# Optimization experiments

Hardware: AMD Instinct MI355X
Metric: run time of the kernel (lower is better)

## Reference

```python
import jax, jax.numpy as jnp
import numpy as np

NEG_SLOPE = 0.2


def gat_layer(x, src, dst, W, a_src, a_dst, bias, num_nodes, concat):
    """PyG-style GATConv (eval mode, self-loops already included in src/dst).
    x: [N, F_in]; W: [F_in, H*C]; a_src, a_dst: [H, C]; bias: [H*C] or [C].
    """
    H, C = a_src.shape
    h = (x @ W).reshape(num_nodes, H, C)                    # [N,H,C]
    alpha_s = jnp.einsum('nhc,hc->nh', h, a_src)            # [N,H]
    alpha_d = jnp.einsum('nhc,hc->nh', h, a_dst)            # [N,H]
    e = alpha_s[src] + alpha_d[dst]                         # [E,H]
    e = jnp.where(e > 0, e, NEG_SLOPE * e)                  # LeakyReLU(0.2)
    # segment softmax over destination nodes (numerically stable)
    m = jax.ops.segment_max(e, dst, num_segments=num_nodes)  # [N,H]
    m = jnp.where(jnp.isfinite(m), m, 0.0)
    ex = jnp.exp(e - m[dst])                                # [E,H]
    s = jax.ops.segment_sum(ex, dst, num_segments=num_nodes)  # [N,H]
    alpha = ex / (s[dst] + 1e-16)                           # [E,H]
    msg = h[src] * alpha[:, :, None]                        # [E,H,C]
    out = jax.ops.segment_sum(msg, dst, num_segments=num_nodes)  # [N,H,C]
    if concat:
        out = out.reshape(num_nodes, H * C)
    else:
        out = out.mean(axis=1)
    return out + bias


def _forward(x, edge_index, W1, a_src1, a_dst1, b1, W2, a_src2, a_dst2, b2):
    N = x.shape[0]
    loops = jnp.arange(N, dtype=edge_index.dtype)
    src = jnp.concatenate([edge_index[0], loops])
    dst = jnp.concatenate([edge_index[1], loops])
    h = gat_layer(x, src, dst, W1, a_src1, a_dst1, b1, N, concat=True)
    h = jax.nn.relu(h)  # dropout inactive in eval
    h = gat_layer(h, src, dst, W2, a_src2, a_dst2, b2, N, concat=False)
    return jax.nn.log_softmax(h, axis=1)


def setup_inputs() -> dict:
    key = jax.random.key(0)
    ks = jax.random.split(key, 10)
    N, E, F_in, Hid, H1, F_out = 100000, 1600000, 128, 64, 2, 7
    x = jax.random.normal(ks[0], (N, F_in), dtype=jnp.float32)
    edge_index = jax.random.randint(ks[1], (2, E), 0, N, dtype=jnp.int64)
    s1 = 1.0 / np.sqrt(F_in)
    W1 = jax.random.uniform(ks[2], (F_in, H1 * Hid), jnp.float32, -s1, s1)
    a_src1 = jax.random.uniform(ks[3], (H1, Hid), jnp.float32, -s1, s1)
    a_dst1 = jax.random.uniform(ks[4], (H1, Hid), jnp.float32, -s1, s1)
    b1 = jnp.zeros((H1 * Hid,), jnp.float32)
    s2 = 1.0 / np.sqrt(H1 * Hid)
    W2 = jax.random.uniform(ks[5], (H1 * Hid, F_out), jnp.float32, -s2, s2)
    a_src2 = jax.random.uniform(ks[6], (1, F_out), jnp.float32, -s2, s2)
    a_dst2 = jax.random.uniform(ks[7], (1, F_out), jnp.float32, -s2, s2)
    b2 = jnp.zeros((F_out,), jnp.float32)
    return {"x": x, "edge_index": edge_index, "W1": W1, "a_src1": a_src1,
            "a_dst1": a_dst1, "b1": b1, "W2": W2, "a_src2": a_src2,
            "a_dst2": a_dst2, "b2": b2}


def reference(x, edge_index, W1, a_src1, a_dst1, b1, W2, a_src2, a_dst2, b2):
    return _forward(x, edge_index, W1, a_src1, a_dst1, b1, W2, a_src2, a_dst2, b2)
```

## Files before the change

### kernel.cpp

```cpp
#include <hip/hip_runtime.h>
#include <hip/hip_bf16.h>

#define F_IN 128
#define HC   128
#define C1   64
#define F_OUT 7
#define H2S  8
#define BSH  9
#define BSZ  512
#define BINCH 8192
#define BCAP 12288

typedef __attribute__((ext_vector_type(8))) short short8;
typedef __attribute__((ext_vector_type(4))) float f32x4;
typedef __attribute__((ext_vector_type(2))) float f32x2;

__device__ __forceinline__ ushort f2bf(float f) {
    uint u = __builtin_bit_cast(uint, f);
    u = (u + 0x7FFFu + ((u >> 16) & 1u)) >> 16;
    return (ushort)u;
}

__device__ __forceinline__ int perm_col(int p_byte) {
    int slp = p_byte >> 3, j = p_byte & 7;
    int h = slp >> 3, sg = slp & 7;
    int lr = 2 * sg + (j >> 2), jj = j & 3;
    return 16 * (4 * h + jj) + lr;
}

__global__ __launch_bounds__(256) void k_bincvt(
    const int* __restrict__ ei, int E, int Etot, int NBIN,
    int* __restrict__ bcnt, uint* __restrict__ binned,
    const float* __restrict__ W1, ushort* __restrict__ Wsw,
    const float* __restrict__ W2, const float* __restrict__ b1,
    float* __restrict__ W2p, float* __restrict__ b1p)
{
    int b = blockIdx.x, t = threadIdx.x;
    if (b < NBIN) {
        __shared__ int hist[256];
        __shared__ int base[256];
        hist[t] = 0;
        __syncthreads();
        long c0 = (long)b * BINCH;
#pragma unroll
        for (int i = 0; i < BINCH / 256; ++i) {
            long e = c0 + t + i * 256;
            if (e < Etot) {
                int d = (e < E) ? ei[E + e] : (int)(e - E);
                atomicAdd(&hist[d >> BSH], 1);
            }
        }
        __syncthreads();
        base[t] = t * BCAP + ((hist[t] > 0) ? atomicAdd(&bcnt[t], hist[t]) : 0);
        __syncthreads();
#pragma unroll
        for (int i = 0; i < BINCH / 256; ++i) {
            long e = c0 + t + i * 256;
            if (e < Etot) {
                int s, d;
                if (e < E) { s = ei[e]; d = ei[E + e]; } else { s = (int)(e - E); d = s; }
                int bkt = d >> BSH;
                int pos = atomicAdd(&base[bkt], 1);
                if (pos < (bkt + 1) * BCAP)
                    binned[pos] = ((uint)s << BSH) | (uint)(d & (BSZ - 1));
            }
        }
    } else if (b < NBIN + 64) {
        int i = (b - NBIN) * 256 + t;
        int k = i >> 7, n = i & 127;
        float v = W1[k * HC + n];
        int idx = n * 128 + (((k & ~7) ^ ((n & 7) << 3)) | (k & 7));
        Wsw[idx] = f2bf(v);
    } else {
        for (int i = t; i < 128 * F_OUT; i += 256) {
            int p = i / F_OUT, o = i - p * F_OUT;
            W2p[i] = W2[perm_col(p) * F_OUT + o];
        }
        if (t < 128) b1p[t] = b1[perm_col(t)];
    }
}

__global__ __launch_bounds__(256) void k_fillgemm(
    const uint* __restrict__ binned, const int* __restrict__ bcnt,
    int* __restrict__ rowptr, int* __restrict__ csr,
    const float* __restrict__ x, const ushort* __restrict__ Wsw,
    const float* __restrict__ a_src, const float* __restrict__ a_dst,
    unsigned char* __restrict__ h1p, float* __restrict__ as1, float* __restrict__ ad1,
    int N, int NB)
{
    __shared__ __align__(16) char smem[128 * 128 * 2];
    const int t = threadIdx.x;

    if ((int)blockIdx.x < NB) {
        int* deg = (int*)smem;
        int* cur = deg + BSZ;
        int* sc  = cur + BSZ;
        int b = blockIdx.x;
        int cv = (t < NB) ? min(bcnt[t], BCAP) : 0;
        sc[t] = cv;
        __syncthreads();
        for (int off = 1; off < 256; off <<= 1) {
            int u = (t >= off) ? sc[t - off] : 0;
            __syncthreads();
            sc[t] += u;
            __syncthreads();
        }
        int total = sc[255];
        int s0 = (b > 0) ? sc[b - 1] : 0;
        int cntb = min(bcnt[b], BCAP);
        __syncthreads();

        int n0 = b << BSH;
        int nn = N - n0; if (nn > BSZ) nn = BSZ;
        deg[t] = 0; deg[t + 256] = 0;
        __syncthreads();
        const uint* bb = binned + (size_t)b * BCAP;
        for (int i = t; i < cntb; i += 256)
            atomicAdd(&deg[bb[i] & (BSZ - 1)], 1);
        __syncthreads();
        int d0 = deg[2 * t], d1 = deg[2 * t + 1];
        int ts = d0 + d1;
        sc[t] = ts;
        __syncthreads();
        for (int off = 1; off < 256; off <<= 1) {
            int u = (t >= off) ? sc[t - off] : 0;
            __syncthreads();
            sc[t] += u;
            __syncthreads();
        }
        int ex = sc[t] - ts + s0;
        if (2 * t < nn)     { rowptr[n0 + 2 * t]     = ex;      cur[2 * t]     = ex; }
        if (2 * t + 1 < nn) { rowptr[n0 + 2 * t + 1] = ex + d0; cur[2 * t + 1] = ex + d0; }
        __syncthreads();
        for (int i = t; i < cntb; i += 256) {
            uint en = bb[i];
            int pos = atomicAdd(&cur[en & (BSZ - 1)], 1);
            csr[pos] = (int)(en >> BSH);
        }
        if (b == 0 && t == 0) rowptr[N] = total;
    } else {
        ushort* Bs = (ushort*)smem;
        const int w = t >> 6, l = t & 63;
        const int lr = l & 15, hi = l >> 4;
        const int n0 = (blockIdx.x - NB) * 64;

        {
            const uint4* src = (const uint4*)Wsw;
            uint4* dst = (uint4*)Bs;
#pragma unroll
            for (int it = 0; it < 8; ++it) dst[t + it * 256] = src[t + it * 256];
        }
        __syncthreads();

        f32x4 acc[8];
#pragma unroll
        for (int j = 0; j < 8; ++j) acc[j] = (f32x4){0.f, 0.f, 0.f, 0.f};

        int arow = n0 + w * 16 + lr;
        if (arow >= N) arow = N - 1;
        const float* aptr = x + (size_t)arow * F_IN + hi * 8;

#pragma unroll
        for (int kt = 0; kt < 4; ++kt) {
            float4 f0 = *(const float4*)(aptr + kt * 32);
            float4 f1 = *(const float4*)(aptr + kt * 32 + 4);
            short8 a;
            a[0] = (short)f2bf(f0.x); a[1] = (short)f2bf(f0.y);
            a[2] = (short)f2bf(f0.z); a[3] = (short)f2bf(f0.w);
            a[4] = (short)f2bf(f1.x); a[5] = (short)f2bf(f1.y);
            a[6] = (short)f2bf(f1.z); a[7] = (short)f2bf(f1.w);
#pragma unroll
            for (int j = 0; j < 8; ++j) {
                int rn = 16 * j + lr;
                int kidx = (kt * 32 + hi * 8) ^ ((rn & 7) << 3);
                short8 b = *(const short8*)(Bs + rn * 128 + kidx);
                acc[j] = __builtin_amdgcn_mfma_f32_16x16x32_bf16(a, b, acc[j], 0, 0, 0);
            }
        }

        float as_[8], ad_[8];
#pragma unroll
        for (int j = 0; j < 8; ++j) {
            int hd = j >> 2;
            int c = 16 * (j & 3) + lr;
            as_[j] = a_src[hd * C1 + c];
            ad_[j] = a_dst[hd * C1 + c];
        }
#pragma unroll
        for (int i = 0; i < 4; ++i) {
            int r = n0 + w * 16 + hi * 4 + i;
            float ps0 = 0, ps1 = 0, pd0 = 0, pd1 = 0;
#pragma unroll
            for (int j = 0; j < 4; ++j) { ps0 += acc[j][i] * as_[j]; pd0 += acc[j][i] * ad_[j]; }
#pragma unroll
            for (int j = 4; j < 8; ++j) { ps1 += acc[j][i] * as_[j]; pd1 += acc[j][i] * ad_[j]; }
#pragma unroll
            for (int off = 1; off <= 8; off <<= 1) {
                ps0 += __shfl_xor(ps0, off, 64);
                ps1 += __shfl_xor(ps1, off, 64);
                pd0 += __shfl_xor(pd0, off, 64);
                pd1 += __shfl_xor(pd1, off, 64);
            }
            if (r < N) {
                int w0 = 0, w1 = 0;
                w0 = __builtin_amdgcn_cvt_pk_fp8_f32(acc[0][i], acc[1][i], w0, false);
                w0 = __builtin_amdgcn_cvt_pk_fp8_f32(acc[2][i], acc[3][i], w0, true);
                w1 = __builtin_amdgcn_cvt_pk_fp8_f32(acc[4][i], acc[5][i], w1, false);
                w1 = __builtin_amdgcn_cvt_pk_fp8_f32(acc[6][i], acc[7][i], w1, true);
                *(uint*)(h1p + (size_t)r * HC + lr * 4)      = (uint)w0;
                *(uint*)(h1p + (size_t)r * HC + 64 + lr * 4) = (uint)w1;
                if (lr == 0) {
                    as1[r * 2 + 0] = ps0; as1[r * 2 + 1] = ps1;
                    ad1[r * 2 + 0] = pd0; ad1[r * 2 + 1] = pd1;
                }
            }
        }
    }
}

__global__ __launch_bounds__(256) void k_aggr1_l2(
    const int* __restrict__ rowptr, const int* __restrict__ csr_src,
    const float* __restrict__ as1, const float* __restrict__ ad1,
    const unsigned char* __restrict__ h1p, const float* __restrict__ b1p,
    const float* __restrict__ W2p, const float* __restrict__ a_src2,
    const float* __restrict__ a_dst2,
    float* __restrict__ h2p, float* __restrict__ as2, float* __restrict__ ad2,
    int N)
{
    int w = threadIdx.x >> 6, l = threadIdx.x & 63;
    int q = l >> 4, sl = l & 15;
    int n = blockIdx.x * 16 + w * 4 + q;
    if (n >= N) return;
    const int h = sl >> 3;
    const int boff = sl * 8;
    float adv = ad1[n * 2 + h];
    int beg = rowptr[n], end = rowptr[n + 1];
    f32x2 ac01 = {0.f, 0.f}, ac23 = {0.f, 0.f}, ac45 = {0.f, 0.f}, ac67 = {0.f, 0.f};
    float s = 0.f;

    int i = beg;
    for (; i + 4 <= end; i += 4) {
        int sv[4]; float Av[4]; uint2 Hv[4];
#pragma unroll
        for (int j = 0; j < 4; ++j) sv[j] = csr_src[i + j];
#pragma unroll
        for (int j = 0; j < 4; ++j) Av[j] = as1[sv[j] * 2 + h];
#pragma unroll
        for (int j = 0; j < 4; ++j)
            Hv[j] = *(const uint2*)(h1p + (((size_t)(uint)sv[j]) << 7) + boff);
#pragma unroll
        for (int j = 0; j < 4; ++j) {
            float a = Av[j] + adv; a = a > 0.f ? a : 0.2f * a;
            float e = __expf(a);
            s += e;
            f32x2 ev = {e, e};
            ac01 += ev * __builtin_amdgcn_cvt_pk_f32_fp8((int)Hv[j].x, false);
            ac23 += ev * __builtin_amdgcn_cvt_pk_f32_fp8((int)Hv[j].x, true);
            ac45 += ev * __builtin_amdgcn_cvt_pk_f32_fp8((int)Hv[j].y, false);
            ac67 += ev * __builtin_amdgcn_cvt_pk_f32_fp8((int)Hv[j].y, true);
        }
    }
    for (; i < end; ++i) {
        int src = csr_src[i];
        float a = as1[src * 2 + h] + adv; a = a > 0.f ? a : 0.2f * a;
        float e = __expf(a);
        s += e;
        uint2 hv = *(const uint2*)(h1p + (((size_t)(uint)src) << 7) + boff);
        f32x2 ev = {e, e};
        ac01 += ev * __builtin_amdgcn_cvt_pk_f32_fp8((int)hv.x, false);
        ac23 += ev * __builtin_amdgcn_cvt_pk_f32_fp8((int)hv.x, true);
        ac45 += ev * __builtin_amdgcn_cvt_pk_f32_fp8((int)hv.y, false);
        ac67 += ev * __builtin_amdgcn_cvt_pk_f32_fp8((int)hv.y, true);
    }
    float inv = 1.f / (s + 1e-16f);

    float4 bv0 = *(const float4*)&b1p[sl * 8];
    float4 bv1 = *(const float4*)&b1p[sl * 8 + 4];
    float v[8];
    v[0] = fmaxf(ac01[0] * inv + bv0.x, 0.f);
    v[1] = fmaxf(ac01[1] * inv + bv0.y, 0.f);
    v[2] = fmaxf(ac23[0] * inv + bv0.z, 0.f);
    v[3] = fmaxf(ac23[1] * inv + bv0.w, 0.f);
    v[4] = fmaxf(ac45[0] * inv + bv1.x, 0.f);
    v[5] = fmaxf(ac45[1] * inv + bv1.y, 0.f);
    v[6] = fmaxf(ac67[0] * inv + bv1.z, 0.f);
    v[7] = fmaxf(ac67[1] * inv + bv1.w, 0.f);

    float w2r[56];
    {
        const float4* wp = (const float4*)(W2p + sl * 56);
#pragma unroll
        for (int k = 0; k < 14; ++k) {
            float4 f = wp[k];
            w2r[4 * k + 0] = f.x; w2r[4 * k + 1] = f.y;
            w2r[4 * k + 2] = f.z; w2r[4 * k + 3] = f.w;
        }
    }
    float p[7];
#pragma unroll
    for (int j = 0; j < 7; ++j) p[j] = 0.f;
#pragma unroll
    for (int r = 0; r < 8; ++r)
#pragma unroll
        for (int j = 0; j < 7; ++j) p[j] += v[r] * w2r[r * 7 + j];
#pragma unroll
    for (int off = 1; off <= 8; off <<= 1)
#pragma unroll
        for (int j = 0; j < 7; ++j) p[j] += __shfl_xor(p[j], off, 64);

    if (sl == 0) {
        float asv = 0.f, adv2 = 0.f;
#pragma unroll
        for (int j = 0; j < 7; ++j) {
            h2p[(size_t)n * H2S + j] = p[j];
            asv += p[j] * a_src2[j];
            adv2 += p[j] * a_dst2[j];
        }
        h2p[(size_t)n * H2S + 7] = 0.f;
        as2[n] = asv; ad2[n] = adv2;
    }
}

__global__ __launch_bounds__(256) void k_aggr2ls(
    const int* __restrict__ rowptr, const int* __restrict__ csr_src,
    const float* __restrict__ as2, const float* __restrict__ ad2,
    const float* __restrict__ h2p, const float* __restrict__ b2,
    float* __restrict__ out, int N)
{
    int g = blockIdx.x * blockDim.x + threadIdx.x;
    int n = g >> 2, l = g & 3;
    if (n >= N) return;
    float adv = ad2[n];
    int beg = rowptr[n], end = rowptr[n + 1];
    f32x2 acc = {0.f, 0.f};
    float s = 0.f;
    int i = beg;
    for (; i + 4 <= end; i += 4) {
        int sv[4]; float Av[4]; float2 Hv[4];
#pragma unroll
        for (int j = 0; j < 4; ++j) sv[j] = csr_src[i + j];
#pragma unroll
        for (int j = 0; j < 4; ++j) Av[j] = as2[sv[j]];
#pragma unroll
        for (int j = 0; j < 4; ++j)
            Hv[j] = *(const float2*)(h2p + ((size_t)(uint)sv[j]) * H2S + 2 * l);
#pragma unroll
        for (int j = 0; j < 4; ++j) {
            float a = Av[j] + adv;
            a = a > 0.f ? a : 0.2f * a;
            float e = __expf(a);
            s += e;
            f32x2 ev = {e, e};
            f32x2 hv = {Hv[j].x, Hv[j].y};
            acc += ev * hv;
        }
    }
    for (; i < end; ++i) {
        int s0 = csr_src[i];
        float a = as2[s0] + adv;
        a = a > 0.f ? a : 0.2f * a;
        float e = __expf(a);
        s += e;
        float2 hv2 = *(const float2*)(h2p + ((size_t)(uint)s0) * H2S + 2 * l);
        f32x2 ev = {e, e};
        f32x2 hv = {hv2.x, hv2.y};
        acc += ev * hv;
    }
    float invs = 1.f / (s + 1e-16f);
    float va = acc[0] * invs + b2[2 * l];
    float vb = (2 * l + 1 < 7) ? acc[1] * invs + b2[2 * l + 1] : -1e30f;
    float m = fmaxf(va, vb);
#pragma unroll
    for (int off = 1; off <= 2; off <<= 1)
        m = fmaxf(m, __shfl_xor(m, off, 4));
    float ex = __expf(va - m) + ((2 * l + 1 < 7) ? __expf(vb - m) : 0.f);
#pragma unroll
    for (int off = 1; off <= 2; off <<= 1)
        ex += __shfl_xor(ex, off, 4);
    float lg = __logf(ex);
    out[(size_t)n * F_OUT + 2 * l] = va - m - lg;
    if (2 * l + 1 < 7) out[(size_t)n * F_OUT + 2 * l + 1] = vb - m - lg;
}

extern "C" void kernel_launch(void* const* d_in, const int* in_sizes, int n_in,
                              void* d_out, int out_size, void* d_ws, size_t ws_size,
                              hipStream_t stream) {
    const float* x      = (const float*)d_in[0];
    const int*   ei     = (const int*)d_in[1];
    const float* W1     = (const float*)d_in[2];
    const float* a_src1 = (const float*)d_in[3];
    const float* a_dst1 = (const float*)d_in[4];
    const float* b1     = (const float*)d_in[5];
    const float* W2     = (const float*)d_in[6];
    const float* a_src2 = (const float*)d_in[7];
    const float* a_dst2 = (const float*)d_in[8];
    const float* b2     = (const float*)d_in[9];
    float* out = (float*)d_out;

    const int N    = in_sizes[0] / F_IN;
    const int E    = in_sizes[1] / 2;
    const int Etot = E + N;
    const int NB   = (N + BSZ - 1) >> BSH;
    const int NBIN = (Etot + BINCH - 1) / BINCH;

    char* ws = (char*)d_ws;
    size_t off = 0;
    auto A = [&](size_t bytes) -> void* {
        char* p = ws + off;
        off += (bytes + 255) & ~(size_t)255;
        return (void*)p;
    };
    ushort* Wsw    = (ushort*)A((size_t)128 * 128 * 2);
    float*  W2p    = (float*) A((size_t)128 * F_OUT * 4);
    float*  b1p    = (float*) A((size_t)128 * 4);
    unsigned char* h1p = (unsigned char*)A((size_t)N * HC);
    float*  as1    = (float*) A((size_t)N * 2 * 4);
    float*  ad1    = (float*) A((size_t)N * 2 * 4);
    int*    rowptr = (int*)   A((size_t)(N + 1) * 4);
    int*    csr    = (int*)   A((size_t)Etot * 4);
    int*    bcnt   = (int*)   A(256 * 4);
    uint*   binned = (uint*)  A((size_t)NB * BCAP * 4);
    float*  h2p    = (float*)binned;
    float*  as2    = (float*)((char*)binned + (((size_t)N * H2S * 4 + 255) & ~(size_t)255));
    float*  ad2    = (float*)((char*)as2 + (((size_t)N * 4 + 255) & ~(size_t)255));

    hipMemsetAsync(bcnt, 0, 256 * 4, stream);

    k_bincvt<<<NBIN + 65, 256, 0, stream>>>(ei, E, Etot, NBIN, bcnt, binned,
                                            W1, Wsw, W2, b1, W2p, b1p);
    k_fillgemm<<<NB + (N + 63) / 64, 256, 0, stream>>>(
        binned, bcnt, rowptr, csr,
        x, Wsw, a_src1, a_dst1, h1p, as1, ad1, N, NB);
    k_aggr1_l2<<<(N + 15) / 16, 256, 0, stream>>>(rowptr, csr, as1, ad1, h1p,
                                                  b1p, W2p, a_src2, a_dst2,
                                                  h2p, as2, ad2, N);
    k_aggr2ls<<<((size_t)N * 4 + 255) / 256, 256, 0, stream>>>(rowptr, csr, as2, ad2,
                                                               h2p, b2, out, N);
}
```

Measured before the change: 147.5 us.

## Sort destination nodes by degree to balance aggregation warps

Builds a degree histogram while constructing the CSR, then a new kernel counting-sorts node ids by in-degree into an order array. Both aggregation kernels process nodes in that order, so the 16-lane groups within a wave handle nodes of similar degree and lose less time to divergent loop lengths. This adds an extra kernel launch, an indirect lookup per node, and scattered writes of outputs that no longer follow node order.

```diff
diff --git a/kernel.cpp b/kernel.cpp
--- a/kernel.cpp
+++ b/kernel.cpp
@@ -10,6 +10,7 @@
 #define BSZ  512
 #define BINCH 8192
 #define BCAP 12288
+#define DBIN 64
 
 typedef __attribute__((ext_vector_type(8))) short short8;
 typedef __attribute__((ext_vector_type(4))) float f32x4;
@@ -82,7 +83,7 @@
 
 __global__ __launch_bounds__(256) void k_fillgemm(
     const uint* __restrict__ binned, const int* __restrict__ bcnt,
-    int* __restrict__ rowptr, int* __restrict__ csr,
+    int* __restrict__ rowptr, int* __restrict__ csr, int* __restrict__ dhist,
     const float* __restrict__ x, const ushort* __restrict__ Wsw,
     const float* __restrict__ a_src, const float* __restrict__ a_dst,
     unsigned char* __restrict__ h1p, float* __restrict__ as1, float* __restrict__ ad1,
@@ -95,9 +96,11 @@
         int* deg = (int*)smem;
         int* cur = deg + BSZ;
         int* sc  = cur + BSZ;
+        int* ldh = sc + 256;
         int b = blockIdx.x;
         int cv = (t < NB) ? min(bcnt[t], BCAP) : 0;
         sc[t] = cv;
+        if (t < DBIN) ldh[t] = 0;
         __syncthreads();
         for (int off = 1; off < 256; off <<= 1) {
             int u = (t >= off) ? sc[t - off] : 0;
@@ -129,9 +132,12 @@
             __syncthreads();
         }
         int ex = sc[t] - ts + s0;
-        if (2 * t < nn)     { rowptr[n0 + 2 * t]     = ex;      cur[2 * t]     = ex; }
-        if (2 * t + 1 < nn) { rowptr[n0 + 2 * t + 1] = ex + d0; cur[2 * t + 1] = ex + d0; }
-        __syncthreads();
+        if (2 * t < nn)     { rowptr[n0 + 2 * t]     = ex;      cur[2 * t]     = ex;
+                              atomicAdd(&ldh[min(d0, DBIN - 1)], 1); }
+        if (2 * t + 1 < nn) { rowptr[n0 + 2 * t + 1] = ex + d0; cur[2 * t + 1] = ex + d0;
+                              atomicAdd(&ldh[min(d1, DBIN - 1)], 1); }
+        __syncthreads();
+        if (t < DBIN && ldh[t]) atomicAdd(&dhist[t], ldh[t]);
         for (int i = t; i < cntb; i += 256) {
             uint en = bb[i];
             int pos = atomicAdd(&cur[en & (BSZ - 1)], 1);
@@ -218,7 +224,38 @@
     }
 }
 
+__global__ __launch_bounds__(256) void k_order(
+    const int* __restrict__ rowptr, const int* __restrict__ dhist,
+    int* __restrict__ dcur, int* __restrict__ order, int N)
+{
+    __shared__ int dstart[DBIN];
+    __shared__ int lh[DBIN];
+    __shared__ int lbase[DBIN];
+    __shared__ int lcur[DBIN];
+    int t = threadIdx.x;
+    if (t == 0) {
+        int a = 0;
+        for (int i = 0; i < DBIN; ++i) { dstart[i] = a; a += dhist[i]; }
+    }
+    if (t < DBIN) { lh[t] = 0; lcur[t] = 0; }
+    __syncthreads();
+    int n = blockIdx.x * 256 + t;
+    int d = -1;
+    if (n < N) {
+        d = min(rowptr[n + 1] - rowptr[n], DBIN - 1);
+        atomicAdd(&lh[d], 1);
+    }
+    __syncthreads();
+    if (t < DBIN && lh[t]) lbase[t] = atomicAdd(&dcur[t], lh[t]);
+    __syncthreads();
+    if (n < N) {
+        int p = atomicAdd(&lcur[d], 1);
+        order[dstart[d] + lbase[d] + p] = n;
+    }
+}
+
 __global__ __launch_bounds__(256) void k_aggr1_l2(
+    const int* __restrict__ order,
     const int* __restrict__ rowptr, const int* __restrict__ csr_src,
     const float* __restrict__ as1, const float* __restrict__ ad1,
     const unsigned char* __restrict__ h1p, const float* __restrict__ b1p,
@@ -229,8 +266,9 @@
 {
     int w = threadIdx.x >> 6, l = threadIdx.x & 63;
     int q = l >> 4, sl = l & 15;
-    int n = blockIdx.x * 16 + w * 4 + q;
-    if (n >= N) return;
+    int idx = blockIdx.x * 16 + w * 4 + q;
+    if (idx >= N) return;
+    int n = order[idx];
     const int h = sl >> 3;
     const int boff = sl * 8;
     float adv = ad1[n * 2 + h];
@@ -322,14 +360,16 @@
 }
 
 __global__ __launch_bounds__(256) void k_aggr2ls(
+    const int* __restrict__ order,
     const int* __restrict__ rowptr, const int* __restrict__ csr_src,
     const float* __restrict__ as2, const float* __restrict__ ad2,
     const float* __restrict__ h2p, const float* __restrict__ b2,
     float* __restrict__ out, int N)
 {
     int g = blockIdx.x * blockDim.x + threadIdx.x;
-    int n = g >> 2, l = g & 3;
-    if (n >= N) return;
+    int idx = g >> 2, l = g & 3;
+    if (idx >= N) return;
+    int n = order[idx];
     float adv = ad2[n];
     int beg = rowptr[n], end = rowptr[n + 1];
     f32x2 acc = {0.f, 0.f};
@@ -418,22 +458,27 @@
     float*  ad1    = (float*) A((size_t)N * 2 * 4);
     int*    rowptr = (int*)   A((size_t)(N + 1) * 4);
     int*    csr    = (int*)   A((size_t)Etot * 4);
-    int*    bcnt   = (int*)   A(256 * 4);
+    int*    order  = (int*)   A((size_t)N * 4);
+    int*    misc   = (int*)   A((256 + DBIN + DBIN) * 4);
+    int*    bcnt   = misc;
+    int*    dhist  = misc + 256;
+    int*    dcur   = misc + 256 + DBIN;
     uint*   binned = (uint*)  A((size_t)NB * BCAP * 4);
     float*  h2p    = (float*)binned;
     float*  as2    = (float*)((char*)binned + (((size_t)N * H2S * 4 + 255) & ~(size_t)255));
     float*  ad2    = (float*)((char*)as2 + (((size_t)N * 4 + 255) & ~(size_t)255));
 
-    hipMemsetAsync(bcnt, 0, 256 * 4, stream);
+    hipMemsetAsync(misc, 0, (256 + DBIN + DBIN) * 4, stream);
 
     k_bincvt<<<NBIN + 65, 256, 0, stream>>>(ei, E, Etot, NBIN, bcnt, binned,
                                             W1, Wsw, W2, b1, W2p, b1p);
     k_fillgemm<<<NB + (N + 63) / 64, 256, 0, stream>>>(
-        binned, bcnt, rowptr, csr,
+        binned, bcnt, rowptr, csr, dhist,
         x, Wsw, a_src1, a_dst1, h1p, as1, ad1, N, NB);
-    k_aggr1_l2<<<(N + 15) / 16, 256, 0, stream>>>(rowptr, csr, as1, ad1, h1p,
+    k_order<<<(N + 255) / 256, 256, 0, stream>>>(rowptr, dhist, dcur, order, N);
+    k_aggr1_l2<<<(N + 15) / 16, 256, 0, stream>>>(order, rowptr, csr, as1, ad1, h1p,
                                                   b1p, W2p, a_src2, a_dst2,
                                                   h2p, as2, ad2, N);
-    k_aggr2ls<<<((size_t)N * 4 + 255) / 256, 256, 0, stream>>>(rowptr, csr, as2, ad2,
-                                                               h2p, b2, out, N);
-}
+    k_aggr2ls<<<((size_t)N * 4 + 255) / 256, 256, 0, stream>>>(order, rowptr, csr,
+                                                               as2, ad2, h2p, b2, out, N);
+}
```

Measured after the change: 157.6 us. 6.9% more time.

## Sort nodes by in-degree within each bin to balance aggregation wavefronts

Applied to the files above, without the earlier changes.

While building the CSR, each 512-node bin counting-sorts its nodes by in-degree (capped at 64 buckets) into an order array. Both aggregation kernels then map lanes to nodes through this order, so nodes with similar degree share a wavefront and divergence in the edge loops drops. The cost is an extra indirection and the loss of contiguous output and dst-feature access, since nodes are now visited in permuted order.

```diff
diff --git a/kernel.cpp b/kernel.cpp
--- a/kernel.cpp
+++ b/kernel.cpp
@@ -10,6 +10,7 @@
 #define BSZ  512
 #define BINCH 8192
 #define BCAP 12288
+#define DBIN 64
 
 typedef __attribute__((ext_vector_type(8))) short short8;
 typedef __attribute__((ext_vector_type(4))) float f32x4;
@@ -82,7 +83,7 @@
 
 __global__ __launch_bounds__(256) void k_fillgemm(
     const uint* __restrict__ binned, const int* __restrict__ bcnt,
-    int* __restrict__ rowptr, int* __restrict__ csr,
+    int* __restrict__ rowptr, int* __restrict__ csr, int* __restrict__ order,
     const float* __restrict__ x, const ushort* __restrict__ Wsw,
     const float* __restrict__ a_src, const float* __restrict__ a_dst,
     unsigned char* __restrict__ h1p, float* __restrict__ as1, float* __restrict__ ad1,
@@ -92,12 +93,16 @@
     const int t = threadIdx.x;
 
     if ((int)blockIdx.x < NB) {
-        int* deg = (int*)smem;
-        int* cur = deg + BSZ;
-        int* sc  = cur + BSZ;
+        int* deg  = (int*)smem;
+        int* cur  = deg + BSZ;
+        int* sc   = cur + BSZ;
+        int* ldh  = sc + 256;
+        int* ldst = ldh + DBIN;
+        int* ldcr = ldst + DBIN;
         int b = blockIdx.x;
         int cv = (t < NB) ? min(bcnt[t], BCAP) : 0;
         sc[t] = cv;
+        if (t < DBIN) { ldh[t] = 0; ldcr[t] = 0; }
         __syncthreads();
         for (int off = 1; off < 256; off <<= 1) {
             int u = (t >= off) ? sc[t - off] : 0;
@@ -129,9 +134,27 @@
             __syncthreads();
         }
         int ex = sc[t] - ts + s0;
-        if (2 * t < nn)     { rowptr[n0 + 2 * t]     = ex;      cur[2 * t]     = ex; }
-        if (2 * t + 1 < nn) { rowptr[n0 + 2 * t + 1] = ex + d0; cur[2 * t + 1] = ex + d0; }
-        __syncthreads();
+        if (2 * t < nn)     { rowptr[n0 + 2 * t]     = ex;      cur[2 * t]     = ex;
+                              atomicAdd(&ldh[min(d0, DBIN - 1)], 1); }
+        if (2 * t + 1 < nn) { rowptr[n0 + 2 * t + 1] = ex + d0; cur[2 * t + 1] = ex + d0;
+                              atomicAdd(&ldh[min(d1, DBIN - 1)], 1); }
+        __syncthreads();
+        if (t == 0) {
+            int a = 0;
+#pragma unroll
+            for (int i = 0; i < DBIN; ++i) { ldst[i] = a; a += ldh[i]; }
+        }
+        __syncthreads();
+        if (2 * t < nn) {
+            int bin = min(d0, DBIN - 1);
+            int p = atomicAdd(&ldcr[bin], 1);
+            order[n0 + ldst[bin] + p] = n0 + 2 * t;
+        }
+        if (2 * t + 1 < nn) {
+            int bin = min(d1, DBIN - 1);
+            int p = atomicAdd(&ldcr[bin], 1);
+            order[n0 + ldst[bin] + p] = n0 + 2 * t + 1;
+        }
         for (int i = t; i < cntb; i += 256) {
             uint en = bb[i];
             int pos = atomicAdd(&cur[en & (BSZ - 1)], 1);
@@ -219,6 +242,7 @@
 }
 
 __global__ __launch_bounds__(256) void k_aggr1_l2(
+    const int* __restrict__ order,
     const int* __restrict__ rowptr, const int* __restrict__ csr_src,
     const float* __restrict__ as1, const float* __restrict__ ad1,
     const unsigned char* __restrict__ h1p, const float* __restrict__ b1p,
@@ -229,8 +253,9 @@
 {
     int w = threadIdx.x >> 6, l = threadIdx.x & 63;
     int q = l >> 4, sl = l & 15;
-    int n = blockIdx.x * 16 + w * 4 + q;
-    if (n >= N) return;
+    int idx = blockIdx.x * 16 + w * 4 + q;
+    if (idx >= N) return;
+    int n = order[idx];
     const int h = sl >> 3;
     const int boff = sl * 8;
     float adv = ad1[n * 2 + h];
@@ -322,14 +347,16 @@
 }
 
 __global__ __launch_bounds__(256) void k_aggr2ls(
+    const int* __restrict__ order,
     const int* __restrict__ rowptr, const int* __restrict__ csr_src,
     const float* __restrict__ as2, const float* __restrict__ ad2,
     const float* __restrict__ h2p, const float* __restrict__ b2,
     float* __restrict__ out, int N)
 {
     int g = blockIdx.x * blockDim.x + threadIdx.x;
-    int n = g >> 2, l = g & 3;
-    if (n >= N) return;
+    int idx = g >> 2, l = g & 3;
+    if (idx >= N) return;
+    int n = order[idx];
     float adv = ad2[n];
     int beg = rowptr[n], end = rowptr[n + 1];
     f32x2 acc = {0.f, 0.f};
@@ -418,6 +445,7 @@
     float*  ad1    = (float*) A((size_t)N * 2 * 4);
     int*    rowptr = (int*)   A((size_t)(N + 1) * 4);
     int*    csr    = (int*)   A((size_t)Etot * 4);
+    int*    order  = (int*)   A((size_t)N * 4);
     int*    bcnt   = (int*)   A(256 * 4);
     uint*   binned = (uint*)  A((size_t)NB * BCAP * 4);
     float*  h2p    = (float*)binned;
@@ -429,11 +457,11 @@
     k_bincvt<<<NBIN + 65, 256, 0, stream>>>(ei, E, Etot, NBIN, bcnt, binned,
                                             W1, Wsw, W2, b1, W2p, b1p);
     k_fillgemm<<<NB + (N + 63) / 64, 256, 0, stream>>>(
-        binned, bcnt, rowptr, csr,
+        binned, bcnt, rowptr, csr, order,
         x, Wsw, a_src1, a_dst1, h1p, as1, ad1, N, NB);
-    k_aggr1_l2<<<(N + 15) / 16, 256, 0, stream>>>(rowptr, csr, as1, ad1, h1p,
+    k_aggr1_l2<<<(N + 15) / 16, 256, 0, stream>>>(order, rowptr, csr, as1, ad1, h1p,
                                                   b1p, W2p, a_src2, a_dst2,
                                                   h2p, as2, ad2, N);
-    k_aggr2ls<<<((size_t)N * 4 + 255) / 256, 256, 0, stream>>>(rowptr, csr, as2, ad2,
-                                                               h2p, b2, out, N);
-}
+    k_aggr2ls<<<((size_t)N * 4 + 255) / 256, 256, 0, stream>>>(order, rowptr, csr,
+                                                               as2, ad2, h2p, b2, out, N);
+}
```

After: 164.9 us. 11.7% more time.

## Regroup kernels so edge binning runs alongside layer-1 GEMM

Applied to the files above, without the earlier changes.

Splits the weight conversion into its own tiny kernel, then fuses edge binning with the x@W1 GEMM in one launch and moves the CSR fill into a separate kernel. Before, binning overlapped only with the cheap weight conversion and the fill overlapped with the GEMM. The new grouping pairs the two larger independent stages, binning and GEMM, so their work can share the GPU. The cost is one extra kernel launch and a now-standalone fill stage with only NB blocks, which may underfill the device.

```diff
diff --git a/kernel.cpp b/kernel.cpp
--- a/kernel.cpp
+++ b/kernel.cpp
@@ -28,20 +28,44 @@
     return 16 * (4 * h + jj) + lr;
 }
 
-__global__ __launch_bounds__(256) void k_bincvt(
-    const int* __restrict__ ei, int E, int Etot, int NBIN,
-    int* __restrict__ bcnt, uint* __restrict__ binned,
+__global__ __launch_bounds__(256) void k_cvt(
     const float* __restrict__ W1, ushort* __restrict__ Wsw,
     const float* __restrict__ W2, const float* __restrict__ b1,
     float* __restrict__ W2p, float* __restrict__ b1p)
 {
     int b = blockIdx.x, t = threadIdx.x;
-    if (b < NBIN) {
-        __shared__ int hist[256];
-        __shared__ int base[256];
+    if (b < 64) {
+        int i = b * 256 + t;
+        int k = i >> 7, n = i & 127;
+        float v = W1[k * HC + n];
+        int idx = n * 128 + (((k & ~7) ^ ((n & 7) << 3)) | (k & 7));
+        Wsw[idx] = f2bf(v);
+    } else {
+        for (int i = t; i < 128 * F_OUT; i += 256) {
+            int p = i / F_OUT, o = i - p * F_OUT;
+            W2p[i] = W2[perm_col(p) * F_OUT + o];
+        }
+        if (t < 128) b1p[t] = b1[perm_col(t)];
+    }
+}
+
+__global__ __launch_bounds__(256) void k_bingemm(
+    const int* __restrict__ ei, int E, int Etot, int NBIN,
+    int* __restrict__ bcnt, uint* __restrict__ binned,
+    const float* __restrict__ x, const ushort* __restrict__ Wsw,
+    const float* __restrict__ a_src, const float* __restrict__ a_dst,
+    unsigned char* __restrict__ h1p, float* __restrict__ as1, float* __restrict__ ad1,
+    int N)
+{
+    __shared__ __align__(16) char smem[128 * 128 * 2];
+    const int t = threadIdx.x;
+
+    if ((int)blockIdx.x < NBIN) {
+        int* hist = (int*)smem;
+        int* base = hist + 256;
         hist[t] = 0;
         __syncthreads();
-        long c0 = (long)b * BINCH;
+        long c0 = (long)blockIdx.x * BINCH;
 #pragma unroll
         for (int i = 0; i < BINCH / 256; ++i) {
             long e = c0 + t + i * 256;
@@ -65,84 +89,11 @@
                     binned[pos] = ((uint)s << BSH) | (uint)(d & (BSZ - 1));
             }
         }
-    } else if (b < NBIN + 64) {
-        int i = (b - NBIN) * 256 + t;
-        int k = i >> 7, n = i & 127;
-        float v = W1[k * HC + n];
-        int idx = n * 128 + (((k & ~7) ^ ((n & 7) << 3)) | (k & 7));
-        Wsw[idx] = f2bf(v);
-    } else {
-        for (int i = t; i < 128 * F_OUT; i += 256) {
-            int p = i / F_OUT, o = i - p * F_OUT;
-            W2p[i] = W2[perm_col(p) * F_OUT + o];
-        }
-        if (t < 128) b1p[t] = b1[perm_col(t)];
-    }
-}
-
-__global__ __launch_bounds__(256) void k_fillgemm(
-    const uint* __restrict__ binned, const int* __restrict__ bcnt,
-    int* __restrict__ rowptr, int* __restrict__ csr,
-    const float* __restrict__ x, const ushort* __restrict__ Wsw,
-    const float* __restrict__ a_src, const float* __restrict__ a_dst,
-    unsigned char* __restrict__ h1p, float* __restrict__ as1, float* __restrict__ ad1,
-    int N, int NB)
-{
-    __shared__ __align__(16) char smem[128 * 128 * 2];
-    const int t = threadIdx.x;
-
-    if ((int)blockIdx.x < NB) {
-        int* deg = (int*)smem;
-        int* cur = deg + BSZ;
-        int* sc  = cur + BSZ;
-        int b = blockIdx.x;
-        int cv = (t < NB) ? min(bcnt[t], BCAP) : 0;
-        sc[t] = cv;
-        __syncthreads();
-        for (int off = 1; off < 256; off <<= 1) {
-            int u = (t >= off) ? sc[t - off] : 0;
-            __syncthreads();
-            sc[t] += u;
-            __syncthreads();
-        }
-        int total = sc[255];
-        int s0 = (b > 0) ? sc[b - 1] : 0;
-        int cntb = min(bcnt[b], BCAP);
-        __syncthreads();
-
-        int n0 = b << BSH;
-        int nn = N - n0; if (nn > BSZ) nn = BSZ;
-        deg[t] = 0; deg[t + 256] = 0;
-        __syncthreads();
-        const uint* bb = binned + (size_t)b * BCAP;
-        for (int i = t; i < cntb; i += 256)
-            atomicAdd(&deg[bb[i] & (BSZ - 1)], 1);
-        __syncthreads();
-        int d0 = deg[2 * t], d1 = deg[2 * t + 1];
-        int ts = d0 + d1;
-        sc[t] = ts;
-        __syncthreads();
-        for (int off = 1; off < 256; off <<= 1) {
-            int u = (t >= off) ? sc[t - off] : 0;
-            __syncthreads();
-            sc[t] += u;
-            __syncthreads();
-        }
-        int ex = sc[t] - ts + s0;
-        if (2 * t < nn)     { rowptr[n0 + 2 * t]     = ex;      cur[2 * t]     = ex; }
-        if (2 * t + 1 < nn) { rowptr[n0 + 2 * t + 1] = ex + d0; cur[2 * t + 1] = ex + d0; }
-        __syncthreads();
-        for (int i = t; i < cntb; i += 256) {
-            uint en = bb[i];
-            int pos = atomicAdd(&cur[en & (BSZ - 1)], 1);
-            csr[pos] = (int)(en >> BSH);
-        }
-        if (b == 0 && t == 0) rowptr[N] = total;
     } else {
         ushort* Bs = (ushort*)smem;
         const int w = t >> 6, l = t & 63;
         const int lr = l & 15, hi = l >> 4;
-        const int n0 = (blockIdx.x - NB) * 64;
+        const int n0 = (blockIdx.x - NBIN) * 64;
 
         {
             const uint4* src = (const uint4*)Wsw;
@@ -216,6 +167,58 @@
             }
         }
     }
+}
+
+__global__ __launch_bounds__(256) void k_fill(
+    const uint* __restrict__ binned, const int* __restrict__ bcnt,
+    int* __restrict__ rowptr, int* __restrict__ csr, int N, int NB)
+{
+    __shared__ int deg[BSZ];
+    __shared__ int cur[BSZ];
+    __shared__ int sc[256];
+    int b = blockIdx.x, t = threadIdx.x;
+    int cv = (t < NB) ? min(bcnt[t], BCAP) : 0;
+    sc[t] = cv;
+    __syncthreads();
+    for (int off = 1; off < 256; off <<= 1) {
+        int u = (t >= off) ? sc[t - off] : 0;
+        __syncthreads();
+        sc[t] += u;
+        __syncthreads();
+    }
+    int total = sc[255];
+    int s0 = (b > 0) ? sc[b - 1] : 0;
+    int cntb = min(bcnt[b], BCAP);
+    __syncthreads();
+
+    int n0 = b << BSH;
+    int nn = N - n0; if (nn > BSZ) nn = BSZ;
+    deg[t] = 0; deg[t + 256] = 0;
+    __syncthreads();
+    const uint* bb = binned + (size_t)b * BCAP;
+    for (int i = t; i < cntb; i += 256)
+        atomicAdd(&deg[bb[i] & (BSZ - 1)], 1);
+    __syncthreads();
+    int d0 = deg[2 * t], d1 = deg[2 * t + 1];
+    int ts = d0 + d1;
+    sc[t] = ts;
+    __syncthreads();
+    for (int off = 1; off < 256; off <<= 1) {
+        int u = (t >= off) ? sc[t - off] : 0;
+        __syncthreads();
+        sc[t] += u;
+        __syncthreads();
+    }
+    int ex = sc[t] - ts + s0;
+    if (2 * t < nn)     { rowptr[n0 + 2 * t]     = ex;      cur[2 * t]     = ex; }
+    if (2 * t + 1 < nn) { rowptr[n0 + 2 * t + 1] = ex + d0; cur[2 * t + 1] = ex + d0; }
+    __syncthreads();
+    for (int i = t; i < cntb; i += 256) {
+        uint en = bb[i];
+        int pos = atomicAdd(&cur[en & (BSZ - 1)], 1);
+        csr[pos] = (int)(en >> BSH);
+    }
+    if (b == 0 && t == 0) rowptr[N] = total;
 }
 
 __global__ __launch_bounds__(256) void k_aggr1_l2(
@@ -426,14 +429,14 @@
 
     hipMemsetAsync(bcnt, 0, 256 * 4, stream);
 
-    k_bincvt<<<NBIN + 65, 256, 0, stream>>>(ei, E, Etot, NBIN, bcnt, binned,
-                                            W1, Wsw, W2, b1, W2p, b1p);
-    k_fillgemm<<<NB + (N + 63) / 64, 256, 0, stream>>>(
-        binned, bcnt, rowptr, csr,
-        x, Wsw, a_src1, a_dst1, h1p, as1, ad1, N, NB);
+    k_cvt<<<65, 256, 0, stream>>>(W1, Wsw, W2, b1, W2p, b1p);
+    k_bingemm<<<NBIN + (N + 63) / 64, 256, 0, stream>>>(
+        ei, E, Etot, NBIN, bcnt, binned,
+        x, Wsw, a_src1, a_dst1, h1p, as1, ad1, N);
+    k_fill<<<NB, 256, 0, stream>>>(binned, bcnt, rowptr, csr, N, NB);
     k_aggr1_l2<<<(N + 15) / 16, 256, 0, stream>>>(rowptr, csr, as1, ad1, h1p,
                                                   b1p, W2p, a_src2, a_dst2,
                                                   h2p, as2, ad2, N);
-    k_aggr2ls<<<((size_t)N * 4 + 255) / 256, 256, 0, stream>>>(rowptr, csr, as2, ad2,
-                                                               h2p, b2, out, N);
-}
+    k_aggr2ls<<<((size_t)N * 4 + 255) / 256, 256, 0, stream>>>(rowptr, csr,
+                                                               as2, ad2, h2p, b2, out, N);
+}
```

Result: no change. 148.9 us (+0.9%).
